# Optimization experiments

Hardware: AMD Instinct MI355X
Metric: run time of the kernel (lower is better)

## Reference

```python
import jax, jax.numpy as jnp
import numpy as np

N_NODES = 100000
N_EDGES = 3200000
IN_C, HID_C, OUT_C = 128, 64, 64


def setup_inputs() -> dict:
    key = jax.random.key(0)
    k = jax.random.split(key, 6)
    x = jax.random.normal(k[0], (N_NODES, IN_C), dtype=jnp.float32)
    edge_index = jax.random.randint(k[1], (2, N_EDGES), 0, N_NODES, dtype=jnp.int64)
    edge_weight = jax.random.uniform(k[2], (N_EDGES,), dtype=jnp.float32)
    W1 = jax.random.normal(k[3], (IN_C, HID_C), dtype=jnp.float32) * (1.0 / np.sqrt(IN_C))
    b1 = jnp.zeros((HID_C,), dtype=jnp.float32)
    W2 = jax.random.normal(k[4], (HID_C, OUT_C), dtype=jnp.float32) * (1.0 / np.sqrt(HID_C))
    b2 = jnp.zeros((OUT_C,), dtype=jnp.float32)
    return {"x": x, "edge_index": edge_index, "edge_weight": edge_weight,
            "W1": W1, "b1": b1, "W2": W2, "b2": b2}


def _gcn_norm(edge_index, edge_weight, num_nodes, dtype):
    # PyG GCNConv default: add self-loops (weight 1), symmetric normalization
    loop = jnp.arange(num_nodes, dtype=edge_index.dtype)
    row = jnp.concatenate([edge_index[0], loop])  # sources
    col = jnp.concatenate([edge_index[1], loop])  # targets (aggregation dim)
    w = jnp.concatenate([edge_weight.astype(dtype), jnp.ones((num_nodes,), dtype)])
    deg = jax.ops.segment_sum(w, col, num_segments=num_nodes)
    deg_inv_sqrt = jnp.where(deg > 0, jax.lax.rsqrt(deg), jnp.zeros((), dtype))
    norm = deg_inv_sqrt[row] * w * deg_inv_sqrt[col]
    return row, col, norm


def _gcn_conv(h, row, col, norm, W, b, num_nodes):
    h = h @ W                      # [N, C_out]
    msg = h[row] * norm[:, None]   # gather over sources, scale by edge norm
    out = jax.ops.segment_sum(msg, col, num_segments=num_nodes)  # scatter-add to targets
    return out + b


def reference(x, edge_index, edge_weight, W1, b1, W2, b2):
    num_nodes = x.shape[0]
    row, col, norm = _gcn_norm(edge_index, edge_weight, num_nodes, x.dtype)
    h = _gcn_conv(x, row, col, norm, W1, b1, num_nodes)
    h = jax.nn.relu(h)
    return _gcn_conv(h, row, col, norm, W2, b2, num_nodes)
```

## Files before the change

kernel.cpp:

```cpp
#include <hip/hip_runtime.h>
#include <hip/hip_bf16.h>

#define N_NODES 100000
#define N_EDGES 3200000
#define IN_C 128
#define HID_C 64
#define OUT_C 64

#define NBUCKET 196
#define SC_EDGES 4096
#define SC_GRID 782
#define CAP 18432
#define MM1_GRID (N_NODES / 16)

struct EdgeRec { int s; float v; };

typedef float f32x2 __attribute__((ext_vector_type(2)));
typedef float f32x4 __attribute__((ext_vector_type(4)));
typedef short bf16x8 __attribute__((ext_vector_type(8)));
union F8 { uint4 u; bf16x8 f; };

__device__ __forceinline__ unsigned pack_bf16(float lo, float hi) {
    unsigned short l = __hip_bfloat16_raw(__float2bfloat16(lo)).x;
    unsigned short h = __hip_bfloat16_raw(__float2bfloat16(hi)).x;
    return ((unsigned)h << 16) | l;
}
__device__ __forceinline__ float bf_lo(unsigned u) {
    union { unsigned u; float f; } c; c.u = u << 16; return c.f;
}
__device__ __forceinline__ float bf_hi(unsigned u) {
    union { unsigned u; float f; } c; c.u = u & 0xffff0000u; return c.f;
}
__device__ __forceinline__ f32x2 bfp(unsigned u) {
    union { unsigned u; float f; } lo, hi;
    lo.u = u << 16; hi.u = u & 0xffff0000u;
    f32x2 r; r.x = lo.f; r.y = hi.f; return r;
}
__device__ __forceinline__ void pk_fma(f32x2& acc, f32x2 a, f32x2 w) {
    asm("v_pk_fma_f32 %0, %1, %2, %0" : "+v"(acc) : "v"(a), "v"(w));
}
__device__ __forceinline__ void edge_acc(f32x2* acc2, uint4 u, float w) {
    f32x2 wv; wv.x = w; wv.y = w;
    pk_fma(acc2[0], bfp(u.x), wv);
    pk_fma(acc2[1], bfp(u.y), wv);
    pk_fma(acc2[2], bfp(u.z), wv);
    pk_fma(acc2[3], bfp(u.w), wv);
}
__device__ __forceinline__ unsigned cvt_pk_bf16(float lo, float hi) {
    unsigned r;
    asm("v_cvt_pk_bf16_f32 %0, %1, %2" : "=v"(r) : "v"(lo), "v"(hi));
    return r;
}
__device__ __forceinline__ void split_frag(const float* f, uint4& hi4, uint4& lo4) {
    unsigned hi[4], lo[4];
    #pragma unroll
    for (int p = 0; p < 4; ++p) {
        hi[p] = cvt_pk_bf16(f[2 * p], f[2 * p + 1]);
        float r0 = f[2 * p]     - bf_lo(hi[p]);
        float r1 = f[2 * p + 1] - bf_hi(hi[p]);
        lo[p] = cvt_pk_bf16(r0, r1);
    }
    hi4 = make_uint4(hi[0], hi[1], hi[2], hi[3]);
    lo4 = make_uint4(lo[0], lo[1], lo[2], lo[3]);
}

__device__ __forceinline__ void scatter_body(const int* __restrict__ ei,
                                             const float* __restrict__ ew,
                                             int* __restrict__ gcursor,
                                             uint2* __restrict__ tmp,
                                             int* hist, int* scn, int* lcur,
                                             int* adj, uint2* rec,
                                             unsigned char* bk) {
    int tid = threadIdx.x;
    hist[tid] = 0;
    __syncthreads();
    int base = blockIdx.x * SC_EDGES;
    unsigned ys[16];
    float    ws[16];
    int      bs[16];
    for (int i = 0; i < 16; ++i) {
        int e = base + i * 256 + tid;
        if (e < N_EDGES) {
            int t = ei[N_EDGES + e];
            bs[i] = t >> 9;
            ys[i] = (unsigned)ei[e] | ((unsigned)(t & 511) << 17);
            ws[i] = ew[e];
            atomicAdd(&hist[bs[i]], 1);
        } else bs[i] = -1;
    }
    __syncthreads();
    int v = hist[tid];
    scn[tid] = v;
    __syncthreads();
    for (int off = 1; off < 256; off <<= 1) {
        int t = scn[tid];
        int add = (tid >= off) ? scn[tid - off] : 0;
        __syncthreads();
        scn[tid] = t + add;
        __syncthreads();
    }
    int excl = scn[tid] - v;
    int gb = (v > 0) ? atomicAdd(&gcursor[tid], v) : 0;
    lcur[tid] = excl;
    adj[tid] = tid * CAP + gb - excl;
    __syncthreads();
    for (int i = 0; i < 16; ++i) {
        if (bs[i] >= 0) {
            int j = atomicAdd(&lcur[bs[i]], 1);
            rec[j] = make_uint2(__float_as_uint(ws[i]), ys[i]);
            bk[j] = (unsigned char)bs[i];
        }
    }
    __syncthreads();
    int count = N_EDGES - base;
    if (count > SC_EDGES) count = SC_EDGES;
    for (int j = tid; j < count; j += 256) {
        int b = bk[j];
        tmp[adj[b] + j] = rec[j];
    }
}

template<int K>
__device__ __forceinline__ void mm_tile_raw(int tile,
                                            const float* __restrict__ X,
                                            const float* __restrict__ W,
                                            float* __restrict__ hf) {
    constexpr int NKS = K / 32;
    int wv = threadIdx.x >> 6;
    int l  = threadIdx.x & 63;
    int lr = l & 15;
    int kr = l >> 4;
    int col = wv * 16 + lr;
    int row0 = tile * 16;
    const float* xbase = X + (size_t)(row0 + lr) * K + kr * 8;
    float4 xa[NKS], xb[NKS];
    #pragma unroll
    for (int ks = 0; ks < NKS; ++ks) {
        const float4* xp = (const float4*)(xbase + ks * 32);
        xa[ks] = xp[0];
        xb[ks] = xp[1];
    }
    F8 bhi[NKS], blo[NKS];
    #pragma unroll
    for (int ks = 0; ks < NKS; ++ks) {
        const float* wp = W + (ks * 32 + kr * 8) * 64 + col;
        float f[8];
        #pragma unroll
        for (int j = 0; j < 8; ++j) f[j] = wp[j * 64];
        split_frag(f, bhi[ks].u, blo[ks].u);
    }
    f32x4 acc = {0.f, 0.f, 0.f, 0.f};
    #pragma unroll
    for (int ks = 0; ks < NKS; ++ks) {
        float f[8] = {xa[ks].x, xa[ks].y, xa[ks].z, xa[ks].w,
                      xb[ks].x, xb[ks].y, xb[ks].z, xb[ks].w};
        F8 ahi, alo;
        split_frag(f, ahi.u, alo.u);
        acc = __builtin_amdgcn_mfma_f32_16x16x32_bf16(ahi.f, bhi[ks].f, acc, 0, 0, 0);
        acc = __builtin_amdgcn_mfma_f32_16x16x32_bf16(ahi.f, blo[ks].f, acc, 0, 0, 0);
        acc = __builtin_amdgcn_mfma_f32_16x16x32_bf16(alo.f, bhi[ks].f, acc, 0, 0, 0);
    }
    int rbase = row0 + kr * 4;
    hf[(size_t)(rbase + 0) * 64 + col] = acc[0];
    hf[(size_t)(rbase + 1) * 64 + col] = acc[1];
    hf[(size_t)(rbase + 2) * 64 + col] = acc[2];
    hf[(size_t)(rbase + 3) * 64 + col] = acc[3];
}

__global__ __launch_bounds__(256) void fused_scatter_mm1(const int* __restrict__ ei,
                                                         const float* __restrict__ ew,
                                                         int* __restrict__ gcursor,
                                                         uint2* __restrict__ tmp,
                                                         const float* __restrict__ x,
                                                         const float* __restrict__ W1,
                                                         float* __restrict__ hf) {
    __shared__ int hist[256];
    __shared__ int scn[256];
    __shared__ int lcur[256];
    __shared__ int adj[256];
    __shared__ uint2 rec[SC_EDGES];
    __shared__ unsigned char bk[SC_EDGES];
    if (blockIdx.x >= SC_GRID) {
        mm_tile_raw<IN_C>(blockIdx.x - SC_GRID, x, W1, hf);
        return;
    }
    scatter_body(ei, ew, gcursor, tmp, hist, scn, lcur, adj, rec, bk);
}

__global__ __launch_bounds__(256) void scatter_coarse(const int* __restrict__ ei,
                                                      const float* __restrict__ ew,
                                                      int* __restrict__ gcursor,
                                                      uint2* __restrict__ tmp) {
    __shared__ int hist[256];
    __shared__ int scn[256];
    __shared__ int lcur[256];
    __shared__ int adj[256];
    __shared__ uint2 rec[SC_EDGES];
    __shared__ unsigned char bk[SC_EDGES];
    scatter_body(ei, ew, gcursor, tmp, hist, scn, lcur, adj, rec, bk);
}

__global__ __launch_bounds__(256) void scalepack(const float* __restrict__ hf,
                                                 const float* __restrict__ dis,
                                                 unsigned* __restrict__ h) {
    int t = blockIdx.x * 256 + threadIdx.x;
    int row = t >> 3, c8 = (t & 7) * 8;
    const float4* p4 = (const float4*)(hf + (size_t)row * 64 + c8);
    float4 f0 = p4[0], f1 = p4[1];
    float d = dis[row];
    uint4 o;
    o.x = pack_bf16(d * f0.x, d * f0.y);
    o.y = pack_bf16(d * f0.z, d * f0.w);
    o.z = pack_bf16(d * f1.x, d * f1.y);
    o.w = pack_bf16(d * f1.z, d * f1.w);
    ((uint4*)h)[(size_t)row * 8 + (t & 7)] = o;
}

template<int K>
__global__ __launch_bounds__(256) void mm_mfma(const float* __restrict__ X,
                                               const float* __restrict__ W,
                                               const float* __restrict__ dis,
                                               unsigned* __restrict__ h) {
    constexpr int NKS = K / 32;
    int wv = threadIdx.x >> 6;
    int l  = threadIdx.x & 63;
    int lr = l & 15;
    int kr = l >> 4;
    int col = wv * 16 + lr;
    F8 bhi[NKS], blo[NKS];
    #pragma unroll
    for (int ks = 0; ks < NKS; ++ks) {
        const float* wp = W + (ks * 32 + kr * 8) * 64 + col;
        float f[8];
        #pragma unroll
        for (int j = 0; j < 8; ++j) f[j] = wp[j * 64];
        split_frag(f, bhi[ks].u, blo[ks].u);
    }
    for (int t = blockIdx.x; t < N_NODES / 16; t += gridDim.x) {
        int row0 = t * 16;
        f32x4 acc = {0.f, 0.f, 0.f, 0.f};
        #pragma unroll
        for (int ks = 0; ks < NKS; ++ks) {
            const float4* xp = (const float4*)(X + (size_t)(row0 + lr) * K + ks * 32 + kr * 8);
            float4 fa = xp[0], fb = xp[1];
            float f[8] = {fa.x, fa.y, fa.z, fa.w, fb.x, fb.y, fb.z, fb.w};
            F8 ahi, alo;
            split_frag(f, ahi.u, alo.u);
            acc = __builtin_amdgcn_mfma_f32_16x16x32_bf16(ahi.f, bhi[ks].f, acc, 0, 0, 0);
            acc = __builtin_amdgcn_mfma_f32_16x16x32_bf16(ahi.f, blo[ks].f, acc, 0, 0, 0);
            acc = __builtin_amdgcn_mfma_f32_16x16x32_bf16(alo.f, bhi[ks].f, acc, 0, 0, 0);
        }
        int rbase = row0 + kr * 4;
        float v0 = acc[0] * dis[rbase + 0];
        float v1 = acc[1] * dis[rbase + 1];
        float v2 = acc[2] * dis[rbase + 2];
        float v3 = acc[3] * dis[rbase + 3];
        float o0 = __shfl_xor(v0, 1, 64);
        float o1 = __shfl_xor(v1, 1, 64);
        float o2 = __shfl_xor(v2, 1, 64);
        float o3 = __shfl_xor(v3, 1, 64);
        if ((lr & 1) == 0) {
            int ci = col >> 1;
            h[(rbase + 0) * 32 + ci] = pack_bf16(v0, o0);
            h[(rbase + 1) * 32 + ci] = pack_bf16(v1, o1);
            h[(rbase + 2) * 32 + ci] = pack_bf16(v2, o2);
            h[(rbase + 3) * 32 + ci] = pack_bf16(v3, o3);
        }
    }
}

__global__ __launch_bounds__(256) void bucket_scan(const int* __restrict__ gcnt,
                                                   int* __restrict__ start) {
    __shared__ int s[256];
    int tid = threadIdx.x;
    int v = gcnt[tid];
    s[tid] = v;
    __syncthreads();
    for (int off = 1; off < 256; off <<= 1) {
        int t = s[tid];
        int add = (tid >= off) ? s[tid - off] : 0;
        __syncthreads();
        s[tid] = t + add;
        __syncthreads();
    }
    start[tid] = s[tid] - v;
    if (tid == 255) start[256] = s[255];
}

__global__ __launch_bounds__(512) void fine_sort(const int* __restrict__ start,
                                                 const uint2* __restrict__ tmpPad,
                                                 int* __restrict__ rowptr,
                                                 float* __restrict__ dis,
                                                 EdgeRec* __restrict__ ed) {
    __shared__ int   cnt[512];
    __shared__ float wdeg[512];
    __shared__ int   s[512];
    int tid = threadIdx.x;
    int nodeBase = blockIdx.x << 9;
    int bb = start[blockIdx.x];
    int nEdge = start[blockIdx.x + 1] - bb;
    const uint2* tb = tmpPad + (size_t)blockIdx.x * CAP;
    cnt[tid] = 0;
    wdeg[tid] = 0.f;
    __syncthreads();
    for (int e = tid; e < nEdge; e += 512) {
        uint2 r = tb[e];
        int l = (r.y >> 17) & 511;
        atomicAdd(&cnt[l], 1);
        atomicAdd(&wdeg[l], __uint_as_float(r.x));
    }
    __syncthreads();
    int v = cnt[tid];
    s[tid] = v;
    __syncthreads();
    for (int off = 1; off < 512; off <<= 1) {
        int t = s[tid];
        int add = (tid >= off) ? s[tid - off] : 0;
        __syncthreads();
        s[tid] = t + add;
        __syncthreads();
    }
    int excl = s[tid] - v;
    int node = nodeBase + tid;
    if (node < N_NODES) {
        rowptr[node] = bb + excl;
        dis[node] = rsqrtf(wdeg[tid] + 1.0f);
    }
    if (node == N_NODES) rowptr[N_NODES] = N_EDGES;
    cnt[tid] = excl;
    __syncthreads();
    for (int e = tid; e < nEdge; e += 512) {
        uint2 r = tb[e];
        int l = (r.y >> 17) & 511;
        int p = atomicAdd(&cnt[l], 1);
        EdgeRec o;
        o.s = (int)(r.y & 0x1FFFFu);
        o.v = __uint_as_float(r.x);
        ed[bb + p] = o;
    }
}

__global__ __launch_bounds__(256, 8) void agg_kernel(const int* __restrict__ rowptr,
                                                     const EdgeRec* __restrict__ ed,
                                                     const unsigned* __restrict__ h,
                                                     const float* __restrict__ dis,
                                                     const float* __restrict__ b,
                                                     float* __restrict__ out,
                                                     int relu) {
    int node = blockIdx.x * 4 + (threadIdx.x >> 6);
    int lane = threadIdx.x & 63;
    int g = lane >> 3;
    int cl = lane & 7;
    int beg = rowptr[node];
    int end = rowptr[node + 1];
    const uint4* h16 = (const uint4*)h;
    const char*  hb  = (const char*)h + (size_t)cl * 16;
    float d  = dis[node];
    uint4 us = h16[(size_t)node * 8 + cl];
    f32x2 acc2[4];
    acc2[0] = 0.f; acc2[1] = 0.f; acc2[2] = 0.f; acc2[3] = 0.f;
    int n = end - beg;
    int nb = (n + 31) >> 5;
    int nm1 = n - 1;
    uint2 q0, q1, q2, q3;
    if (nb > 0) {
        q0 = *(const uint2*)(ed + beg + min(g,      nm1));
        q1 = *(const uint2*)(ed + beg + min(g + 8,  nm1));
        q2 = *(const uint2*)(ed + beg + min(g + 16, nm1));
        q3 = *(const uint2*)(ed + beg + min(g + 24, nm1));
        for (int bt = 0; bt < nb; ++bt) {
            int ob = (bt << 5) + g;
            float w0 = (ob      < n) ? __uint_as_float(q0.y) : 0.f;
            float w1 = (ob + 8  < n) ? __uint_as_float(q1.y) : 0.f;
            float w2 = (ob + 16 < n) ? __uint_as_float(q2.y) : 0.f;
            float w3 = (ob + 24 < n) ? __uint_as_float(q3.y) : 0.f;
            uint4 u0 = *(const uint4*)(hb + ((size_t)(unsigned)q0.x << 7));
            uint4 u1 = *(const uint4*)(hb + ((size_t)(unsigned)q1.x << 7));
            uint4 u2 = *(const uint4*)(hb + ((size_t)(unsigned)q2.x << 7));
            uint4 u3 = *(const uint4*)(hb + ((size_t)(unsigned)q3.x << 7));
            if (bt + 1 < nb) {
                int on = ob + 32;
                q0 = *(const uint2*)(ed + beg + min(on,      nm1));
                q1 = *(const uint2*)(ed + beg + min(on + 8,  nm1));
                q2 = *(const uint2*)(ed + beg + min(on + 16, nm1));
                q3 = *(const uint2*)(ed + beg + min(on + 24, nm1));
            }
            edge_acc(acc2, u0, w0);
            edge_acc(acc2, u1, w1);
            edge_acc(acc2, u2, w2);
            edge_acc(acc2, u3, w3);
        }
    }
    float acc[8] = { acc2[0].x, acc2[0].y, acc2[1].x, acc2[1].y,
                     acc2[2].x, acc2[2].y, acc2[3].x, acc2[3].y };
    #pragma unroll
    for (int kk = 0; kk < 8; ++kk) {
        acc[kk] += __shfl_xor(acc[kk], 8, 64);
        acc[kk] += __shfl_xor(acc[kk], 16, 64);
        acc[kk] += __shfl_xor(acc[kk], 32, 64);
    }
    if (g == 0) {
        float hs[8] = { bf_lo(us.x), bf_hi(us.x), bf_lo(us.y), bf_hi(us.y),
                        bf_lo(us.z), bf_hi(us.z), bf_lo(us.w), bf_hi(us.w) };
        const float4* b4 = (const float4*)b;
        float4 bv0 = b4[cl * 2], bv1 = b4[cl * 2 + 1];
        float4 v0, v1;
        v0.x = d * (acc[0] + hs[0]) + bv0.x;
        v0.y = d * (acc[1] + hs[1]) + bv0.y;
        v0.z = d * (acc[2] + hs[2]) + bv0.z;
        v0.w = d * (acc[3] + hs[3]) + bv0.w;
        v1.x = d * (acc[4] + hs[4]) + bv1.x;
        v1.y = d * (acc[5] + hs[5]) + bv1.y;
        v1.z = d * (acc[6] + hs[6]) + bv1.z;
        v1.w = d * (acc[7] + hs[7]) + bv1.w;
        if (relu) {
            v0.x = fmaxf(v0.x, 0.f); v0.y = fmaxf(v0.y, 0.f);
            v0.z = fmaxf(v0.z, 0.f); v0.w = fmaxf(v0.w, 0.f);
            v1.x = fmaxf(v1.x, 0.f); v1.y = fmaxf(v1.y, 0.f);
            v1.z = fmaxf(v1.z, 0.f); v1.w = fmaxf(v1.w, 0.f);
        }
        float4* o4 = (float4*)out;
        o4[node * 16 + cl * 2]     = v0;
        o4[node * 16 + cl * 2 + 1] = v1;
    }
}

extern "C" void kernel_launch(void* const* d_in, const int* in_sizes, int n_in,
                              void* d_out, int out_size, void* d_ws, size_t ws_size,
                              hipStream_t stream) {
    const float* x  = (const float*)d_in[0];
    const int*   ei = (const int*)d_in[1];
    const float* ew = (const float*)d_in[2];
    const float* W1 = (const float*)d_in[3];
    const float* b1 = (const float*)d_in[4];
    const float* W2 = (const float*)d_in[5];
    const float* b2 = (const float*)d_in[6];
    float* out = (float*)d_out;

    char* p = (char*)d_ws;
    auto carve = [&](size_t bytes) { char* r = p; p += (bytes + 255) & ~(size_t)255; return r; };
    int*      rowptr  = (int*)carve((N_NODES + 1) * 4);
    int*      start   = (int*)carve(257 * 4);
    int*      gcursor = (int*)carve(256 * 4);
    float*    dis     = (float*)carve(N_NODES * 4);
    EdgeRec*  ed      = (EdgeRec*)carve((size_t)N_EDGES * 8);
    unsigned* h       = (unsigned*)carve((size_t)N_NODES * 64 * 2);

    size_t tmpsz = (size_t)NBUCKET * CAP * 8;
    size_t hfsz  = (size_t)N_NODES * 64 * 4;
    size_t used  = (size_t)(p - (char*)d_ws);
    bool fast = ws_size >= used + hfsz + tmpsz + 512;

    if (fast) {
        float* hf     = (float*)carve(hfsz);
        uint2* tmpPad = (uint2*)carve(tmpsz);
        float* a      = hf;

        hipMemsetAsync(gcursor, 0, 256 * sizeof(int), stream);
        fused_scatter_mm1<<<SC_GRID + MM1_GRID, 256, 0, stream>>>(ei, ew, gcursor,
                                                                  tmpPad, x, W1, hf);
        bucket_scan<<<1, 256, 0, stream>>>(gcursor, start);
        fine_sort<<<NBUCKET, 512, 0, stream>>>(start, tmpPad, rowptr, dis, ed);
        scalepack<<<N_NODES * 8 / 256, 256, 0, stream>>>(hf, dis, h);
        agg_kernel<<<N_NODES / 4, 256, 0, stream>>>(rowptr, ed, h, dis, b1, a, 1);
        mm_mfma<HID_C><<<1250, 256, 0, stream>>>(a, W2, dis, h);
        agg_kernel<<<N_NODES / 4, 256, 0, stream>>>(rowptr, ed, h, dis, b2, out, 0);
    } else {
        size_t asz = (size_t)N_NODES * 64 * 4;
        char*  r2  = carve(tmpsz > asz ? tmpsz : asz);
        uint2* tmpPad = (uint2*)r2;
        float* a      = (float*)r2;

        hipMemsetAsync(gcursor, 0, 256 * sizeof(int), stream);
        scatter_coarse<<<SC_GRID, 256, 0, stream>>>(ei, ew, gcursor, tmpPad);
        bucket_scan<<<1, 256, 0, stream>>>(gcursor, start);
        fine_sort<<<NBUCKET, 512, 0, stream>>>(start, tmpPad, rowptr, dis, ed);
        mm_mfma<IN_C><<<1250, 256, 0, stream>>>(x, W1, dis, h);
        agg_kernel<<<N_NODES / 4, 256, 0, stream>>>(rowptr, ed, h, dis, b1, a, 1);
        mm_mfma<HID_C><<<1250, 256, 0, stream>>>(a, W2, dis, h);
        agg_kernel<<<N_NODES / 4, 256, 0, stream>>>(rowptr, ed, h, dis, b2, out, 0);
    }
}
```

Baseline: 357.1 us.

## Fuse scalepack into fine_sort, emit split-bf16 activations, halve scatter chunk

```diff
diff --git a/kernel.cpp b/kernel.cpp
--- a/kernel.cpp
+++ b/kernel.cpp
@@ -8,8 +8,9 @@
 #define OUT_C 64
 
 #define NBUCKET 196
-#define SC_EDGES 4096
-#define SC_GRID 782
+#define SC_EDGES 2048
+#define SC_PER   (SC_EDGES / 256)
+#define SC_GRID  1563
 #define CAP 18432
 #define MM1_GRID (N_NODES / 16)
 
@@ -75,10 +76,10 @@
     hist[tid] = 0;
     __syncthreads();
     int base = blockIdx.x * SC_EDGES;
-    unsigned ys[16];
-    float    ws[16];
-    int      bs[16];
-    for (int i = 0; i < 16; ++i) {
+    unsigned ys[SC_PER];
+    float    ws[SC_PER];
+    int      bs[SC_PER];
+    for (int i = 0; i < SC_PER; ++i) {
         int e = base + i * 256 + tid;
         if (e < N_EDGES) {
             int t = ei[N_EDGES + e];
@@ -104,7 +105,7 @@
     lcur[tid] = excl;
     adj[tid] = tid * CAP + gb - excl;
     __syncthreads();
-    for (int i = 0; i < 16; ++i) {
+    for (int i = 0; i < SC_PER; ++i) {
         if (bs[i] >= 0) {
             int j = atomicAdd(&lcur[bs[i]], 1);
             rec[j] = make_uint2(__float_as_uint(ws[i]), ys[i]);
@@ -200,22 +201,6 @@
     scatter_body(ei, ew, gcursor, tmp, hist, scn, lcur, adj, rec, bk);
 }
 
-__global__ __launch_bounds__(256) void scalepack(const float* __restrict__ hf,
-                                                 const float* __restrict__ dis,
-                                                 unsigned* __restrict__ h) {
-    int t = blockIdx.x * 256 + threadIdx.x;
-    int row = t >> 3, c8 = (t & 7) * 8;
-    const float4* p4 = (const float4*)(hf + (size_t)row * 64 + c8);
-    float4 f0 = p4[0], f1 = p4[1];
-    float d = dis[row];
-    uint4 o;
-    o.x = pack_bf16(d * f0.x, d * f0.y);
-    o.y = pack_bf16(d * f0.z, d * f0.w);
-    o.z = pack_bf16(d * f1.x, d * f1.y);
-    o.w = pack_bf16(d * f1.z, d * f1.w);
-    ((uint4*)h)[(size_t)row * 8 + (t & 7)] = o;
-}
-
 template<int K>
 __global__ __launch_bounds__(256) void mm_mfma(const float* __restrict__ X,
                                                const float* __restrict__ W,
@@ -269,6 +254,55 @@
     }
 }
 
+__global__ __launch_bounds__(256) void mm2_bf(const unsigned* __restrict__ A,
+                                              const float* __restrict__ W,
+                                              const float* __restrict__ dis,
+                                              unsigned* __restrict__ h) {
+    int wv = threadIdx.x >> 6;
+    int l  = threadIdx.x & 63;
+    int lr = l & 15;
+    int kr = l >> 4;
+    int col = wv * 16 + lr;
+    int row0 = blockIdx.x * 16;
+    const uint4* a4 = (const uint4*)A;
+    size_t rb = (size_t)(row0 + lr) * 16;
+    F8 ah0, al0, ah1, al1;
+    ah0.u = a4[rb + kr];          al0.u = a4[rb + 8 + kr];
+    ah1.u = a4[rb + 4 + kr];      al1.u = a4[rb + 12 + kr];
+    F8 bhi[2], blo[2];
+    #pragma unroll
+    for (int ks = 0; ks < 2; ++ks) {
+        const float* wp = W + (ks * 32 + kr * 8) * 64 + col;
+        float f[8];
+        #pragma unroll
+        for (int j = 0; j < 8; ++j) f[j] = wp[j * 64];
+        split_frag(f, bhi[ks].u, blo[ks].u);
+    }
+    f32x4 acc = {0.f, 0.f, 0.f, 0.f};
+    acc = __builtin_amdgcn_mfma_f32_16x16x32_bf16(ah0.f, bhi[0].f, acc, 0, 0, 0);
+    acc = __builtin_amdgcn_mfma_f32_16x16x32_bf16(ah0.f, blo[0].f, acc, 0, 0, 0);
+    acc = __builtin_amdgcn_mfma_f32_16x16x32_bf16(al0.f, bhi[0].f, acc, 0, 0, 0);
+    acc = __builtin_amdgcn_mfma_f32_16x16x32_bf16(ah1.f, bhi[1].f, acc, 0, 0, 0);
+    acc = __builtin_amdgcn_mfma_f32_16x16x32_bf16(ah1.f, blo[1].f, acc, 0, 0, 0);
+    acc = __builtin_amdgcn_mfma_f32_16x16x32_bf16(al1.f, bhi[1].f, acc, 0, 0, 0);
+    int rbase = row0 + kr * 4;
+    float v0 = acc[0] * dis[rbase + 0];
+    float v1 = acc[1] * dis[rbase + 1];
+    float v2 = acc[2] * dis[rbase + 2];
+    float v3 = acc[3] * dis[rbase + 3];
+    float o0 = __shfl_xor(v0, 1, 64);
+    float o1 = __shfl_xor(v1, 1, 64);
+    float o2 = __shfl_xor(v2, 1, 64);
+    float o3 = __shfl_xor(v3, 1, 64);
+    if ((lr & 1) == 0) {
+        int ci = col >> 1;
+        h[(rbase + 0) * 32 + ci] = pack_bf16(v0, o0);
+        h[(rbase + 1) * 32 + ci] = pack_bf16(v1, o1);
+        h[(rbase + 2) * 32 + ci] = pack_bf16(v2, o2);
+        h[(rbase + 3) * 32 + ci] = pack_bf16(v3, o3);
+    }
+}
+
 __global__ __launch_bounds__(256) void bucket_scan(const int* __restrict__ gcnt,
                                                    int* __restrict__ start) {
     __shared__ int s[256];
@@ -291,7 +325,9 @@
                                                  const uint2* __restrict__ tmpPad,
                                                  int* __restrict__ rowptr,
                                                  float* __restrict__ dis,
-                                                 EdgeRec* __restrict__ ed) {
+                                                 EdgeRec* __restrict__ ed,
+                                                 const float* __restrict__ hf,
+                                                 unsigned* __restrict__ h) {
     __shared__ int   cnt[512];
     __shared__ float wdeg[512];
     __shared__ int   s[512];
@@ -338,6 +374,23 @@
         o.v = __uint_as_float(r.x);
         ed[bb + p] = o;
     }
+    if (hf) {
+        int nNode = N_NODES - nodeBase;
+        if (nNode > 512) nNode = 512;
+        uint4* h4 = (uint4*)h;
+        for (int i = tid; i < nNode * 8; i += 512) {
+            int r = i >> 3;
+            float d = rsqrtf(wdeg[r] + 1.0f);
+            const float4* pf = (const float4*)(hf + ((size_t)(nodeBase + r)) * 64 + (i & 7) * 8);
+            float4 f0 = pf[0], f1 = pf[1];
+            uint4 o;
+            o.x = pack_bf16(d * f0.x, d * f0.y);
+            o.y = pack_bf16(d * f0.z, d * f0.w);
+            o.z = pack_bf16(d * f1.x, d * f1.y);
+            o.w = pack_bf16(d * f1.z, d * f1.w);
+            h4[(size_t)nodeBase * 8 + i] = o;
+        }
+    }
 }
 
 __global__ __launch_bounds__(256, 8) void agg_kernel(const int* __restrict__ rowptr,
@@ -346,7 +399,7 @@
                                                      const float* __restrict__ dis,
                                                      const float* __restrict__ b,
                                                      float* __restrict__ out,
-                                                     int relu) {
+                                                     int relu, int packa) {
     int node = blockIdx.x * 4 + (threadIdx.x >> 6);
     int lane = threadIdx.x & 63;
     int g = lane >> 3;
@@ -404,24 +457,33 @@
                         bf_lo(us.z), bf_hi(us.z), bf_lo(us.w), bf_hi(us.w) };
         const float4* b4 = (const float4*)b;
         float4 bv0 = b4[cl * 2], bv1 = b4[cl * 2 + 1];
-        float4 v0, v1;
-        v0.x = d * (acc[0] + hs[0]) + bv0.x;
-        v0.y = d * (acc[1] + hs[1]) + bv0.y;
-        v0.z = d * (acc[2] + hs[2]) + bv0.z;
-        v0.w = d * (acc[3] + hs[3]) + bv0.w;
-        v1.x = d * (acc[4] + hs[4]) + bv1.x;
-        v1.y = d * (acc[5] + hs[5]) + bv1.y;
-        v1.z = d * (acc[6] + hs[6]) + bv1.z;
-        v1.w = d * (acc[7] + hs[7]) + bv1.w;
+        float vv[8];
+        vv[0] = d * (acc[0] + hs[0]) + bv0.x;
+        vv[1] = d * (acc[1] + hs[1]) + bv0.y;
+        vv[2] = d * (acc[2] + hs[2]) + bv0.z;
+        vv[3] = d * (acc[3] + hs[3]) + bv0.w;
+        vv[4] = d * (acc[4] + hs[4]) + bv1.x;
+        vv[5] = d * (acc[5] + hs[5]) + bv1.y;
+        vv[6] = d * (acc[6] + hs[6]) + bv1.z;
+        vv[7] = d * (acc[7] + hs[7]) + bv1.w;
         if (relu) {
-            v0.x = fmaxf(v0.x, 0.f); v0.y = fmaxf(v0.y, 0.f);
-            v0.z = fmaxf(v0.z, 0.f); v0.w = fmaxf(v0.w, 0.f);
-            v1.x = fmaxf(v1.x, 0.f); v1.y = fmaxf(v1.y, 0.f);
-            v1.z = fmaxf(v1.z, 0.f); v1.w = fmaxf(v1.w, 0.f);
-        }
-        float4* o4 = (float4*)out;
-        o4[node * 16 + cl * 2]     = v0;
-        o4[node * 16 + cl * 2 + 1] = v1;
+            #pragma unroll
+            for (int kk = 0; kk < 8; ++kk) vv[kk] = fmaxf(vv[kk], 0.f);
+        }
+        if (packa) {
+            uint4 hi4, lo4;
+            split_frag(vv, hi4, lo4);
+            uint4* ab = (uint4*)out;
+            ab[(size_t)node * 16 + cl]     = hi4;
+            ab[(size_t)node * 16 + 8 + cl] = lo4;
+        } else {
+            float4 v0, v1;
+            v0.x = vv[0]; v0.y = vv[1]; v0.z = vv[2]; v0.w = vv[3];
+            v1.x = vv[4]; v1.y = vv[5]; v1.z = vv[6]; v1.w = vv[7];
+            float4* o4 = (float4*)out;
+            o4[node * 16 + cl * 2]     = v0;
+            o4[node * 16 + cl * 2 + 1] = v1;
+        }
     }
 }
 
@@ -452,32 +514,34 @@
     bool fast = ws_size >= used + hfsz + tmpsz + 512;
 
     if (fast) {
-        float* hf     = (float*)carve(hfsz);
-        uint2* tmpPad = (uint2*)carve(tmpsz);
-        float* a      = hf;
+        float*    hf     = (float*)carve(hfsz);
+        uint2*    tmpPad = (uint2*)carve(tmpsz);
+        unsigned* a      = (unsigned*)hf;
 
         hipMemsetAsync(gcursor, 0, 256 * sizeof(int), stream);
         fused_scatter_mm1<<<SC_GRID + MM1_GRID, 256, 0, stream>>>(ei, ew, gcursor,
                                                                   tmpPad, x, W1, hf);
         bucket_scan<<<1, 256, 0, stream>>>(gcursor, start);
-        fine_sort<<<NBUCKET, 512, 0, stream>>>(start, tmpPad, rowptr, dis, ed);
-        scalepack<<<N_NODES * 8 / 256, 256, 0, stream>>>(hf, dis, h);
-        agg_kernel<<<N_NODES / 4, 256, 0, stream>>>(rowptr, ed, h, dis, b1, a, 1);
-        mm_mfma<HID_C><<<1250, 256, 0, stream>>>(a, W2, dis, h);
-        agg_kernel<<<N_NODES / 4, 256, 0, stream>>>(rowptr, ed, h, dis, b2, out, 0);
+        fine_sort<<<NBUCKET, 512, 0, stream>>>(start, tmpPad, rowptr, dis, ed, hf, h);
+        agg_kernel<<<N_NODES / 4, 256, 0, stream>>>(rowptr, ed, h, dis, b1,
+                                                    (float*)a, 1, 1);
+        mm2_bf<<<N_NODES / 16, 256, 0, stream>>>(a, W2, dis, h);
+        agg_kernel<<<N_NODES / 4, 256, 0, stream>>>(rowptr, ed, h, dis, b2, out, 0, 0);
     } else {
         size_t asz = (size_t)N_NODES * 64 * 4;
         char*  r2  = carve(tmpsz > asz ? tmpsz : asz);
-        uint2* tmpPad = (uint2*)r2;
-        float* a      = (float*)r2;
+        uint2*    tmpPad = (uint2*)r2;
+        unsigned* a      = (unsigned*)r2;
 
         hipMemsetAsync(gcursor, 0, 256 * sizeof(int), stream);
         scatter_coarse<<<SC_GRID, 256, 0, stream>>>(ei, ew, gcursor, tmpPad);
         bucket_scan<<<1, 256, 0, stream>>>(gcursor, start);
-        fine_sort<<<NBUCKET, 512, 0, stream>>>(start, tmpPad, rowptr, dis, ed);
+        fine_sort<<<NBUCKET, 512, 0, stream>>>(start, tmpPad, rowptr, dis, ed,
+                                               (const float*)nullptr, (unsigned*)nullptr);
         mm_mfma<IN_C><<<1250, 256, 0, stream>>>(x, W1, dis, h);
-        agg_kernel<<<N_NODES / 4, 256, 0, stream>>>(rowptr, ed, h, dis, b1, a, 1);
-        mm_mfma<HID_C><<<1250, 256, 0, stream>>>(a, W2, dis, h);
-        agg_kernel<<<N_NODES / 4, 256, 0, stream>>>(rowptr, ed, h, dis, b2, out, 0);
-    }
-}
+        agg_kernel<<<N_NODES / 4, 256, 0, stream>>>(rowptr, ed, h, dis, b1,
+                                                    (float*)a, 1, 1);
+        mm2_bf<<<N_NODES / 16, 256, 0, stream>>>(a, W2, dis, h);
+        agg_kernel<<<N_NODES / 4, 256, 0, stream>>>(rowptr, ed, h, dis, b2, out, 0, 0);
+    }
+}
```

After: 374.0 us. 1.05x slower.
